# Performance work log

Hardware: AMD Instinct MI355X
Metric: run time of the kernel (lower is better)

## Reference

```python
import jax, jax.numpy as jnp
import numpy as np

N_NODES = 50000
N_EDGES = 600000
D = 128


def gcn_conv(x, src, dst, W, b, n_nodes):
    """PyG GCNConv: h = D^-1/2 (A+I) D^-1/2 (x @ W) + b, messages src->dst."""
    h = x @ W  # [N, out]
    # add self loops (weight 1)
    loop = jnp.arange(n_nodes, dtype=src.dtype)
    s = jnp.concatenate([src, loop])
    d = jnp.concatenate([dst, loop])
    w = jnp.ones(s.shape[0], dtype=x.dtype)
    deg = jax.ops.segment_sum(w, d, num_segments=n_nodes)  # in-degree at target
    dinv = jnp.where(deg > 0, jax.lax.rsqrt(deg), 0.0).astype(x.dtype)
    norm = dinv[s] * w * dinv[d]  # [E+N]
    msg = h[s] * norm[:, None]  # gather + scale
    out = jax.ops.segment_sum(msg, d, num_segments=n_nodes)  # scatter-add
    return out + b


def setup_inputs() -> dict:
    key = jax.random.key(0)
    k1, k2, k3, k4, k5, k6 = jax.random.split(key, 6)
    x = jax.random.normal(k1, (N_NODES, D), dtype=jnp.float32)
    edge_index = jax.random.randint(k2, (2, N_EDGES), 0, N_NODES, dtype=jnp.int64)
    s = (1.0 / np.sqrt(D))
    W1 = jax.random.normal(k3, (D, D), dtype=jnp.float32) * s
    b1 = jnp.zeros((D,), dtype=jnp.float32)
    W2 = jax.random.normal(k4, (D, D), dtype=jnp.float32) * s
    b2 = jnp.zeros((D,), dtype=jnp.float32)
    return {"x": x, "edge_index": edge_index, "W1": W1, "b1": b1, "W2": W2, "b2": b2}


def reference(x, edge_index, W1, b1, W2, b2):
    src, dst = edge_index[0], edge_index[1]
    # two GCN layers (order=2), ReLU activation; dropout is identity at eval
    o1 = jax.nn.relu(gcn_conv(x, src, dst, W1, b1, N_NODES))
    o2 = jax.nn.relu(gcn_conv(x, src, dst, W2, b2, N_NODES))
    # combine_mode='mean'
    return 0.5 * (o1 + o2)
```

## Files before the change

kernel.cpp:

```cpp
#include <hip/hip_runtime.h>
#include <hip/hip_bf16.h>

#define N_NODES 50000
#define N_EDGES 600000
#define D 128
#define CAP 64
#define ZSTRIDE 136

typedef __attribute__((ext_vector_type(8))) short bfrag;
typedef __attribute__((ext_vector_type(4))) float ffrag;

__device__ __forceinline__ short bf16bits(float f) {
    __hip_bfloat16 h = __float2bfloat16(f);
    return *reinterpret_cast<short*>(&h);
}

__device__ __forceinline__ unsigned norm_cnt(unsigned raw) {
    return raw - (raw >= 0x80000000u ? 0xAAAAAAAAu : 0u);
}

__global__ void fill_kernel(const int* __restrict__ src, const int* __restrict__ dst,
                            unsigned* __restrict__ cnt, int* __restrict__ srcs) {
    int e = blockIdx.x * 256 + threadIdx.x;
    if (e < N_EDGES) {
        int d = dst[e];
        unsigned slot = norm_cnt(atomicAdd(&cnt[d], 1u));
        if (slot < CAP) srcs[d * CAP + slot] = src[e];
    }
}

__global__ __launch_bounds__(256) void dxw_kernel(
    const float* __restrict__ x,
    const float* __restrict__ W1, const float* __restrict__ W2,
    const unsigned* __restrict__ cnt,
    float* __restrict__ dinv,
    __hip_bfloat162* __restrict__ xs, int* __restrict__ srcs,
    short* __restrict__ wpack)
{
    int idx = blockIdx.x * 256 + threadIdx.x;

    int node = idx >> 6;
    unsigned deg = norm_cnt(cnt[node]);
    float dv = rsqrtf((float)(deg + 1));
    float2 v = ((const float2*)x)[idx];
    __hip_bfloat162 h;
    h.x = __float2bfloat16(dv * v.x);
    h.y = __float2bfloat16(dv * v.y);
    xs[idx] = h;

    if ((idx & 63) == 0) {
        dinv[node] = dv;
        unsigned n8 = (deg + 7u) & ~7u;
        n8 = n8 < CAP ? n8 : CAP;
        for (unsigned s2 = deg; s2 < n8; ++s2) srcs[node * CAP + s2] = N_NODES;
    }

    if (idx < 64) {
        __hip_bfloat162 z0;
        z0.x = __float2bfloat16(0.f);
        z0.y = __float2bfloat16(0.f);
        xs[N_NODES * 64 + idx] = z0;
    }

    if (idx < 2 * 8 * 4 * 64 * 8) {
        int j  = idx & 7;
        int l  = (idx >> 3) & 63;
        int ks = (idx >> 9) & 3;
        int c  = (idx >> 11) & 7;
        int m  = (idx >> 14) & 1;
        int k = ks * 32 + (l >> 4) * 8 + j;
        int n = c * 16 + (l & 15);
        const float* W = m ? W2 : W1;
        wpack[idx] = bf16bits(W[k * D + n]);
    }
}

__global__ __launch_bounds__(256, 5) void fused_kernel(
    const float* __restrict__ x,
    const unsigned* __restrict__ cnt,
    const int* __restrict__ srcs,
    const float* __restrict__ dinv,
    const __hip_bfloat162* __restrict__ xs,
    const short* __restrict__ wpack,
    const float* __restrict__ b1,
    const float* __restrict__ b2,
    float* __restrict__ out)
{
    __shared__ __align__(16) short zs16[16 * ZSTRIDE];
    const int base = blockIdx.x * 16;
    const int t = threadIdx.x;
    const int lane = t & 63;
    const int f2 = lane;
    const int g = t >> 6;

    for (int rr = 0; rr < 4; ++rr) {
        const int r = g * 4 + rr;
        const int node = base + r;
        unsigned deg = norm_cnt(cnt[node]);
        unsigned n8 = (deg + 7u) & ~7u;
        n8 = n8 < CAP ? n8 : CAP;
        const int rowbase = node * CAP;
        const float dv = dinv[node];
        float ax[8], ay[8];
#pragma unroll
        for (int j = 0; j < 8; ++j) { ax[j] = 0.f; ay[j] = 0.f; }
        for (unsigned e = 0; e < n8; e += 8) {
#pragma unroll
            for (int j = 0; j < 8; ++j) {
                int s = srcs[rowbase + e + j];
                __hip_bfloat162 h = xs[s * 64 + f2];
                ax[j] += __bfloat162float(h.x);
                ay[j] += __bfloat162float(h.y);
            }
        }
        float sx = ((ax[0] + ax[1]) + (ax[2] + ax[3])) + ((ax[4] + ax[5]) + (ax[6] + ax[7]));
        float sy = ((ay[0] + ay[1]) + (ay[2] + ay[3])) + ((ay[4] + ay[5]) + (ay[6] + ay[7]));
        float2 xv = ((const float2*)x)[node * 64 + f2];
        __hip_bfloat162 z;
        z.x = __float2bfloat16(dv * (sx + dv * xv.x));
        z.y = __float2bfloat16(dv * (sy + dv * xv.y));
        *(__hip_bfloat162*)&zs16[r * ZSTRIDE + 2 * f2] = z;
    }
    __syncthreads();

    const int m16 = lane & 15;
    const int quad = lane >> 4;
    const int c0 = 2 * g;
    const int c1 = 2 * g + 1;

    ffrag acc00 = {0.f, 0.f, 0.f, 0.f};
    ffrag acc01 = {0.f, 0.f, 0.f, 0.f};
    ffrag acc10 = {0.f, 0.f, 0.f, 0.f};
    ffrag acc11 = {0.f, 0.f, 0.f, 0.f};

#pragma unroll
    for (int ks = 0; ks < 4; ++ks) {
        bfrag a = *(const bfrag*)&zs16[m16 * ZSTRIDE + ks * 32 + quad * 8];

        bfrag b00 = *(const bfrag*)&wpack[((((0 * 8 + c0) * 4 + ks) * 64 + lane) * 8)];
        bfrag b01 = *(const bfrag*)&wpack[((((0 * 8 + c1) * 4 + ks) * 64 + lane) * 8)];
        bfrag b10 = *(const bfrag*)&wpack[((((1 * 8 + c0) * 4 + ks) * 64 + lane) * 8)];
        bfrag b11 = *(const bfrag*)&wpack[((((1 * 8 + c1) * 4 + ks) * 64 + lane) * 8)];

        acc00 = __builtin_amdgcn_mfma_f32_16x16x32_bf16(a, b00, acc00, 0, 0, 0);
        acc01 = __builtin_amdgcn_mfma_f32_16x16x32_bf16(a, b01, acc01, 0, 0, 0);
        acc10 = __builtin_amdgcn_mfma_f32_16x16x32_bf16(a, b10, acc10, 0, 0, 0);
        acc11 = __builtin_amdgcn_mfma_f32_16x16x32_bf16(a, b11, acc11, 0, 0, 0);
    }

    const int n0 = c0 * 16 + m16;
    const int n1 = c1 * 16 + m16;
    const float b1n0 = b1[n0], b1n1 = b1[n1];
    const float b2n0 = b2[n0], b2n1 = b2[n1];
#pragma unroll
    for (int reg = 0; reg < 4; ++reg) {
        int row = quad * 4 + reg;
        int node = base + row;
        float o0 = 0.5f * (fmaxf(acc00[reg] + b1n0, 0.f) + fmaxf(acc10[reg] + b2n0, 0.f));
        float o1 = 0.5f * (fmaxf(acc01[reg] + b1n1, 0.f) + fmaxf(acc11[reg] + b2n1, 0.f));
        out[node * D + n0] = o0;
        out[node * D + n1] = o1;
    }
}

extern "C" void kernel_launch(void* const* d_in, const int* in_sizes, int n_in,
                              void* d_out, int out_size, void* d_ws, size_t ws_size,
                              hipStream_t stream) {
    const float* x  = (const float*)d_in[0];
    const int*   ei = (const int*)d_in[1];
    const float* W1 = (const float*)d_in[2];
    const float* b1 = (const float*)d_in[3];
    const float* W2 = (const float*)d_in[4];
    const float* b2 = (const float*)d_in[5];
    float* out = (float*)d_out;

    const int* src = ei;
    const int* dst = ei + N_EDGES;

    char* ws = (char*)d_ws;
    unsigned* cnt  = (unsigned*)(ws + 0);
    float*    dinv = (float*)(ws + 200704);
    int*      srcs = (int*)(ws + 401408);
    __hip_bfloat162* xs = (__hip_bfloat162*)(ws + 13201408);
    short*    wpack = (short*)(ws + 26001664);

    fill_kernel<<<(N_EDGES + 255) / 256, 256, 0, stream>>>(src, dst, cnt, srcs);
    dxw_kernel<<<12500, 256, 0, stream>>>(x, W1, W2, cnt, dinv, xs, srcs, wpack);
    fused_kernel<<<N_NODES / 16, 256, 0, stream>>>(x, cnt, srcs, dinv, xs, wpack,
                                                   b1, b2, out);
}
```

Measured before the change: 155.2 us.

## Gather neighbor rows with 16-byte loads split across lane quarters, drop dinv and x reads

The aggregation loop is restructured so each quarter of the wavefront loads a different neighbor's row with 16-byte bf16 vector loads, then partial sums are combined with cross-lane shuffles. Before, every lane issued a 4-byte load per neighbor. The self-loop term now reuses the pre-scaled bf16 xs row instead of rereading fp32 x, and dinv is recomputed from the count rather than stored and loaded. This cuts memory traffic and the number of load instructions, at the cost of shuffle reductions and only a quarter of the lanes writing the result. Using bf16 for the self-loop term adds a little rounding error.

```diff
diff --git a/kernel.cpp b/kernel.cpp
--- a/kernel.cpp
+++ b/kernel.cpp
@@ -13,6 +13,10 @@
 __device__ __forceinline__ short bf16bits(float f) {
     __hip_bfloat16 h = __float2bfloat16(f);
     return *reinterpret_cast<short*>(&h);
+}
+__device__ __forceinline__ float bfbits2float(short b) {
+    unsigned u = ((unsigned)(unsigned short)b) << 16;
+    return __uint_as_float(u);
 }
 
 __device__ __forceinline__ unsigned norm_cnt(unsigned raw) {
@@ -33,7 +37,6 @@
     const float* __restrict__ x,
     const float* __restrict__ W1, const float* __restrict__ W2,
     const unsigned* __restrict__ cnt,
-    float* __restrict__ dinv,
     __hip_bfloat162* __restrict__ xs, int* __restrict__ srcs,
     short* __restrict__ wpack)
 {
@@ -49,7 +52,6 @@
     xs[idx] = h;
 
     if ((idx & 63) == 0) {
-        dinv[node] = dv;
         unsigned n8 = (deg + 7u) & ~7u;
         n8 = n8 < CAP ? n8 : CAP;
         for (unsigned s2 = deg; s2 < n8; ++s2) srcs[node * CAP + s2] = N_NODES;
@@ -76,10 +78,8 @@
 }
 
 __global__ __launch_bounds__(256, 5) void fused_kernel(
-    const float* __restrict__ x,
     const unsigned* __restrict__ cnt,
     const int* __restrict__ srcs,
-    const float* __restrict__ dinv,
     const __hip_bfloat162* __restrict__ xs,
     const short* __restrict__ wpack,
     const float* __restrict__ b1,
@@ -90,36 +90,47 @@
     const int base = blockIdx.x * 16;
     const int t = threadIdx.x;
     const int lane = t & 63;
-    const int f2 = lane;
     const int g = t >> 6;
+    const int p = lane & 15;
+    const int q = lane >> 4;
 
     for (int rr = 0; rr < 4; ++rr) {
         const int r = g * 4 + rr;
         const int node = base + r;
         unsigned deg = norm_cnt(cnt[node]);
+        const float dv = rsqrtf((float)(deg + 1));
         unsigned n8 = (deg + 7u) & ~7u;
         n8 = n8 < CAP ? n8 : CAP;
-        const int rowbase = node * CAP;
-        const float dv = dinv[node];
-        float ax[8], ay[8];
-#pragma unroll
-        for (int j = 0; j < 8; ++j) { ax[j] = 0.f; ay[j] = 0.f; }
+        const int rb = node * CAP;
+
+        float acc[8];
+#pragma unroll
+        for (int j = 0; j < 8; ++j) acc[j] = 0.f;
+
         for (unsigned e = 0; e < n8; e += 8) {
-#pragma unroll
-            for (int j = 0; j < 8; ++j) {
-                int s = srcs[rowbase + e + j];
-                __hip_bfloat162 h = xs[s * 64 + f2];
-                ax[j] += __bfloat162float(h.x);
-                ay[j] += __bfloat162float(h.y);
-            }
+            int s0 = srcs[rb + e + q];
+            int s1 = srcs[rb + e + 4 + q];
+            bfrag v0 = ((const bfrag*)(xs + s0 * 64))[p];
+            bfrag v1 = ((const bfrag*)(xs + s1 * 64))[p];
+#pragma unroll
+            for (int j = 0; j < 8; ++j)
+                acc[j] += bfbits2float(v0[j]) + bfbits2float(v1[j]);
         }
-        float sx = ((ax[0] + ax[1]) + (ax[2] + ax[3])) + ((ax[4] + ax[5]) + (ax[6] + ax[7]));
-        float sy = ((ay[0] + ay[1]) + (ay[2] + ay[3])) + ((ay[4] + ay[5]) + (ay[6] + ay[7]));
-        float2 xv = ((const float2*)x)[node * 64 + f2];
-        __hip_bfloat162 z;
-        z.x = __float2bfloat16(dv * (sx + dv * xv.x));
-        z.y = __float2bfloat16(dv * (sy + dv * xv.y));
-        *(__hip_bfloat162*)&zs16[r * ZSTRIDE + 2 * f2] = z;
+
+#pragma unroll
+        for (int j = 0; j < 8; ++j) {
+            acc[j] += __shfl_xor(acc[j], 16, 64);
+            acc[j] += __shfl_xor(acc[j], 32, 64);
+        }
+
+        if (q == 0) {
+            bfrag vs = ((const bfrag*)(xs + node * 64))[p];
+            bfrag zo;
+#pragma unroll
+            for (int j = 0; j < 8; ++j)
+                zo[j] = bf16bits(dv * (acc[j] + bfbits2float(vs[j])));
+            *(bfrag*)&zs16[r * ZSTRIDE + p * 8] = zo;
+        }
     }
     __syncthreads();
 
@@ -179,13 +190,11 @@
 
     char* ws = (char*)d_ws;
     unsigned* cnt  = (unsigned*)(ws + 0);
-    float*    dinv = (float*)(ws + 200704);
-    int*      srcs = (int*)(ws + 401408);
-    __hip_bfloat162* xs = (__hip_bfloat162*)(ws + 13201408);
-    short*    wpack = (short*)(ws + 26001664);
+    int*      srcs = (int*)(ws + 200704);
+    __hip_bfloat162* xs = (__hip_bfloat162*)(ws + 13000704);
+    short*    wpack = (short*)(ws + 25800960);
 
     fill_kernel<<<(N_EDGES + 255) / 256, 256, 0, stream>>>(src, dst, cnt, srcs);
-    dxw_kernel<<<12500, 256, 0, stream>>>(x, W1, W2, cnt, dinv, xs, srcs, wpack);
-    fused_kernel<<<N_NODES / 16, 256, 0, stream>>>(x, cnt, srcs, dinv, xs, wpack,
-                                                   b1, b2, out);
-}
+    dxw_kernel<<<12500, 256, 0, stream>>>(x, W1, W2, cnt, xs, srcs, wpack);
+    fused_kernel<<<N_NODES / 16, 256, 0, stream>>>(cnt, srcs, xs, wpack, b1, b2, out);
+}
```

New measurement: 155.0 us. Within noise of the previous version (-0.1%).
